# Optimization experiments

Measured on AMD Instinct MI355X. Metric: run time of the kernel, lower is better.

Reference implementation:

```python
import jax, jax.numpy as jnp
import numpy as np

B, S, D, H, HD, E, DE = 2, 512, 768, 12, 64, 50, 50  # batch, seq, input_dim, heads, head_dim, edge_dim, dep_embed_dim


def setup_inputs() -> dict:
    key = jax.random.key(0)
    ks = jax.random.split(key, 16)
    def xn(k, shape, s=0.02):
        return (jax.random.normal(k, shape, jnp.float32) * s)
    return {
        'weight_prob_softmax': jax.random.uniform(ks[0], (B, S, S, E), jnp.float32),
        'weight_adj': jax.random.normal(ks[1], (B, S, S, E), jnp.float32),
        'gcn_inputs': jax.random.normal(ks[2], (B, S, D), jnp.float32),
        'self_loop': jax.random.uniform(ks[3], (B, S, S, E), jnp.float32),
        # self.linear
        'W_lin': xn(ks[4], (D, D)), 'b_lin': jnp.zeros((D,), jnp.float32),
        # additive attention vectors fc_w1 / fc_w2 (stored [H, HD])
        'fc_w1': xn(ks[5], (H, HD), 0.2), 'fc_w2': xn(ks[6], (H, HD), 0.2),
        # edge_mlp: Linear(E,128) -> ReLU -> (Dropout eval) -> Linear(128,H)
        'We1': xn(ks[7], (128, E), 0.1), 'be1': jnp.zeros((128,), jnp.float32),
        'We2': xn(ks[8], (H, 128), 0.1), 'be2': jnp.zeros((H,), jnp.float32),
        # self.W output projection
        'W_out': xn(ks[9], (D, D)), 'b_out': jnp.zeros((D,), jnp.float32),
        # LayerNorm params
        'ln_a': jnp.ones((D,), jnp.float32), 'ln_b': jnp.zeros((D,), jnp.float32),
        # highway.W split into column blocks: [edge | edge_i | edge_j | node1 | node2]
        'Wh_e': xn(ks[10], (DE, E), 0.1), 'Wh_ei': xn(ks[11], (DE, E), 0.1),
        'Wh_ej': xn(ks[12], (DE, E), 0.1), 'Wh_n1': xn(ks[13], (DE, D), 0.05),
        'Wh_n2': xn(ks[14], (DE, D), 0.05), 'bh': jnp.zeros((DE,), jnp.float32),
    }


def reference(weight_prob_softmax, weight_adj, gcn_inputs, self_loop,
              W_lin, b_lin, fc_w1, fc_w2, We1, be1, We2, be2,
              W_out, b_out, ln_a, ln_b, Wh_e, Wh_ei, Wh_ej, Wh_n1, Wh_n2, bh):
    wps = self_loop + weight_prob_softmax                      # [B,S,S,E]
    mask = jnp.sum(wps, axis=-1) == 0.0                        # [B,S,S]
    feature = (gcn_inputs @ W_lin.T + b_lin).reshape(B, S, H, HD)
    attn_src = jnp.einsum('bshd,hd->bhs', feature, fc_w1)      # [B,H,S]
    attn_dst = jnp.einsum('bshd,hd->bhs', feature, fc_w2)      # [B,H,S]
    # edge MLP bias (dropout is identity in eval)
    hmid = jax.nn.relu(jnp.einsum('bije,fe->bijf', wps, We1) + be1)  # [B,S,S,128]
    A = jnp.einsum('bijf,hf->bhij', hmid, We2) + be2[None, :, None, None]  # [B,H,S,S]
    attn = jax.nn.leaky_relu(attn_src[:, :, :, None] + attn_dst[:, :, None, :] + A,
                             negative_slope=0.01)
    attn = jnp.where(mask[:, None, :, :], -jnp.inf, attn)
    attn = jax.nn.softmax(attn, axis=-1)
    gcn = jnp.einsum('bhij,bjhd->bihd', attn, feature).reshape(B, S, D)
    gcn = gcn @ W_out.T + b_out
    # torch LayerNorm variant: unbiased std, divide by (std + eps)
    mean = jnp.mean(gcn, axis=-1, keepdims=True)
    std = jnp.std(gcn, axis=-1, ddof=1, keepdims=True)
    gcn = ln_a * (gcn - mean) / (std + 1e-6) + ln_b
    node = jax.nn.relu(gcn)                                    # [B,S,D]
    # RefiningStrategy: W([edge, edge_i, edge_j, node1, node2]) via block matmuls
    ediag = jnp.diagonal(weight_adj, axis1=1, axis2=2).transpose(0, 2, 1)  # [B,S,E]
    edge_out = (jnp.einsum('bije,fe->bijf', weight_adj, Wh_e)
                + (ediag @ Wh_ei.T)[:, :, None, :]             # edge_i[b,i,j]=diag[b,i]
                + (ediag @ Wh_ej.T)[:, None, :, :]             # edge_j[b,i,j]=diag[b,j]
                + (node @ Wh_n1.T)[:, None, :, :]              # node1[b,i,j]=node[b,j]
                + (node @ Wh_n2.T)[:, :, None, :]              # node2[b,i,j]=node[b,i]
                + bh)                                          # [B,S,S,DE]
    return node, edge_out
```

## Files before the change

### kernel.cpp

```cpp
#include <hip/hip_runtime.h>
#include <math.h>
#include <stddef.h>

#define BB 2
#define SS 512
#define DD 768
#define HH 12
#define HDIM 64
#define EE 50
#define DE 50
#define F1 128

typedef float f32x4 __attribute__((ext_vector_type(4)));
typedef short s16x8 __attribute__((ext_vector_type(8)));

static __device__ __forceinline__ unsigned short f2bf(float x) {
  unsigned int u = __float_as_uint(x);
  unsigned int r = u + 0x7fffu + ((u >> 16) & 1u);
  return (unsigned short)(r >> 16);
}
static __device__ __forceinline__ float bf2f(unsigned short b) {
  return __uint_as_float(((unsigned int)b) << 16);
}

__global__ __launch_bounds__(256) void k_gemm_bias(
    const float* __restrict__ X, int ldx,
    const float* __restrict__ W,
    const float* __restrict__ bias,
    float* __restrict__ Y, int ldy,
    int M, int N, int K)
{
  __shared__ float Xs[32][68];
  __shared__ float Ws[32][68];
  int t = threadIdx.x;
  int tx = t & 15, ty = t >> 4;
  int m0 = blockIdx.y * 64, n0 = blockIdx.x * 64;
  float acc[4][4] = {};
  for (int k0 = 0; k0 < K; k0 += 32) {
#pragma unroll
    for (int q = 0; q < 2; ++q) {
      int idx = t + q * 256;
      int r = idx >> 3, c = (idx & 7) << 2;
      float4 v = *(const float4*)(X + (size_t)(m0 + r) * ldx + k0 + c);
      Xs[c + 0][r] = v.x; Xs[c + 1][r] = v.y; Xs[c + 2][r] = v.z; Xs[c + 3][r] = v.w;
      float4 w = *(const float4*)(W + (size_t)(n0 + r) * K + k0 + c);
      Ws[c + 0][r] = w.x; Ws[c + 1][r] = w.y; Ws[c + 2][r] = w.z; Ws[c + 3][r] = w.w;
    }
    __syncthreads();
#pragma unroll
    for (int kk = 0; kk < 32; ++kk) {
      float a[4], b[4];
#pragma unroll
      for (int u = 0; u < 4; ++u) a[u] = Xs[kk][ty * 4 + u];
#pragma unroll
      for (int u = 0; u < 4; ++u) b[u] = Ws[kk][tx * 4 + u];
#pragma unroll
      for (int i = 0; i < 4; ++i)
#pragma unroll
        for (int j = 0; j < 4; ++j) acc[i][j] += a[i] * b[j];
    }
    __syncthreads();
  }
#pragma unroll
  for (int i = 0; i < 4; ++i) {
    int m = m0 + ty * 4 + i;
#pragma unroll
    for (int j = 0; j < 4; ++j) {
      int n = n0 + tx * 4 + j;
      Y[(size_t)m * ldy + n] = acc[i][j] + bias[n];
    }
  }
}

__global__ __launch_bounds__(192) void k_attnvec(
    const float* __restrict__ feat, const float* __restrict__ w1,
    const float* __restrict__ w2, float* __restrict__ src, float* __restrict__ dst)
{
  int bs = blockIdx.x;
  int t = threadIdx.x;
  int h = t >> 4, l = t & 15;
  float4 f = *(const float4*)(feat + (size_t)bs * DD + h * HDIM + l * 4);
  float4 a = *(const float4*)(w1 + h * HDIM + l * 4);
  float4 c = *(const float4*)(w2 + h * HDIM + l * 4);
  float ps = f.x * a.x + f.y * a.y + f.z * a.z + f.w * a.w;
  float pd = f.x * c.x + f.y * c.y + f.z * c.z + f.w * c.w;
#pragma unroll
  for (int o = 8; o > 0; o >>= 1) {
    ps += __shfl_xor(ps, o);
    pd += __shfl_xor(pd, o);
  }
  if (l == 0) {
    int b = bs >> 9, s = bs & 511;
    src[((b * HH + h) << 9) + s] = ps;
    dst[((b * HH + h) << 9) + s] = pd;
  }
}

__global__ __launch_bounds__(64) void k_prep(
    const float* __restrict__ We1, const float* __restrict__ be1,
    const float* __restrict__ We2, const float* __restrict__ Whe,
    s16x8* __restrict__ wtab, float* __restrict__ betab,
    s16x8* __restrict__ wtabE)
{
  const int l = threadIdx.x;
  const int lr = l & 15, lg = l >> 4;
#pragma unroll
  for (int ks = 0; ks < 2; ++ks)
#pragma unroll
    for (int n = 0; n < 8; ++n) {
      s16x8 v;
#pragma unroll
      for (int u = 0; u < 8; ++u) {
        int e = ks * 32 + lg * 8 + u;
        float x = (e < 50) ? We1[(n * 16 + lr) * 50 + e] : 0.0f;
        v[u] = (short)f2bf(x);
      }
      wtab[(ks * 8 + n) * 64 + l] = v;
    }
#pragma unroll
  for (int kk = 0; kk < 4; ++kk) {
    s16x8 v;
#pragma unroll
    for (int u = 0; u < 8; ++u) {
      int f = kk * 32 + lg * 8 + u;
      v[u] = (short)((lr < 12) ? f2bf(We2[lr * 128 + f]) : (unsigned short)0);
    }
    wtab[(16 + kk) * 64 + l] = v;
  }
#pragma unroll
  for (int n = 0; n < 8; ++n) betab[n * 64 + l] = be1[n * 16 + lr];
#pragma unroll
  for (int nt = 0; nt < 4; ++nt)
#pragma unroll
    for (int ks = 0; ks < 2; ++ks) {
      int f = nt * 16 + lr;
      s16x8 v;
#pragma unroll
      for (int u = 0; u < 8; ++u) {
        int e = ks * 32 + lg * 8 + u;
        float x = (f < 50 && e < 50) ? Whe[f * 50 + e] : 0.0f;
        v[u] = (short)f2bf(x);
      }
      wtabE[(nt * 2 + ks) * 64 + l] = v;
    }
}

__global__ __launch_bounds__(256, 2) void k_fused_attn(
    const float* __restrict__ wprob, const float* __restrict__ sloop,
    const s16x8* __restrict__ wtab, const float* __restrict__ betab,
    const float* __restrict__ be2,
    const float* __restrict__ src, const float* __restrict__ dst,
    const float* __restrict__ feat, float* __restrict__ gout)
{
  __shared__ float p[2][12][512];
  __shared__ unsigned short hmid_s[128][72];
  __shared__ float masks[128];

  const int blk = blockIdx.x;
  const int b = blk >> 8;
  const int i0 = (blk & 255) << 1;
  const int t = threadIdx.x;
  const int w = t >> 6, l = t & 63;
  const int lr = l & 15, lg = l >> 4;
  const int jbase = w * 32;

  s16x8 wb[4];
#pragma unroll
  for (int kk = 0; kk < 4; ++kk) wb[kk] = wtab[(16 + kk) * 64 + l];
  float be1v[8];
#pragma unroll
  for (int n = 0; n < 8; ++n) be1v[n] = betab[n * 64 + l];
  const int hc = (lr < 12) ? lr : 0;
  const float be2v = be2[hc];
  const float srcv_[2] = {src[((b * HH + hc) << 9) + i0],
                          src[((b * HH + hc) << 9) + i0 + 1]};
  const float* drow = dst + ((size_t)(b * HH + hc) << 9);

  int offs[8];
  bool vmask[8];
#pragma unroll
  for (int s8 = 0; s8 < 8; ++s8) {
    int ks = s8 >> 2, q = s8 & 3;
    int off = ks * 32 + lg * 8 + 2 * q;
    vmask[s8] = (off <= 48);
    offs[s8] = vmask[s8] ? off : 0;
  }

#pragma unroll 2
  for (int it = 0; it < 8; ++it) {
    const int ii = it >> 2, c = it & 3;
    const int i = i0 + ii;
    const int j0c = c << 7;

    const size_t rowbase = ((size_t)(b * SS + i) * SS + j0c) * EE;
    float2 pA[2][8], pS[2][8];
#pragma unroll
    for (int jt = 0; jt < 2; ++jt) {
      const int jl = jbase + jt * 16 + lr;
      const float* wrow = wprob + rowbase + (size_t)jl * EE;
      const float* srow = sloop + rowbase + (size_t)jl * EE;
#pragma unroll
      for (int s8 = 0; s8 < 8; ++s8) {
        pA[jt][s8] = *(const float2*)(wrow + offs[s8]);
        pS[jt][s8] = *(const float2*)(srow + offs[s8]);
      }
    }
    float4 dv0 = *(const float4*)(drow + j0c + jbase + lg * 4);
    float4 dv1 = *(const float4*)(drow + j0c + jbase + 16 + lg * 4);

    s16x8 aA[2][2];
    float rsum[2];
#pragma unroll
    for (int jt = 0; jt < 2; ++jt) {
      float rs = 0.0f;
#pragma unroll
      for (int ks = 0; ks < 2; ++ks) {
        s16x8 f;
#pragma unroll
        for (int q = 0; q < 4; ++q) {
          int s8 = ks * 4 + q;
          float vx = vmask[s8] ? (pA[jt][s8].x + pS[jt][s8].x) : 0.0f;
          float vy = vmask[s8] ? (pA[jt][s8].y + pS[jt][s8].y) : 0.0f;
          f[2 * q] = (short)f2bf(vx);
          f[2 * q + 1] = (short)f2bf(vy);
          rs += vx + vy;
        }
        aA[jt][ks] = f;
      }
      rsum[jt] = rs;
    }
#pragma unroll
    for (int jt = 0; jt < 2; ++jt) {
      rsum[jt] += __shfl_xor(rsum[jt], 16);
      rsum[jt] += __shfl_xor(rsum[jt], 32);
    }
    if (lg == 0) {
      masks[jbase + lr] = (rsum[0] == 0.0f) ? 1.0f : 0.0f;
      masks[jbase + 16 + lr] = (rsum[1] == 0.0f) ? 1.0f : 0.0f;
    }

    f32x4 accB[2] = {};
#pragma unroll
    for (int h = 0; h < 2; ++h) {
      s16x8 wah[2][4];
#pragma unroll
      for (int ks = 0; ks < 2; ++ks)
#pragma unroll
        for (int nn = 0; nn < 4; ++nn)
          wah[ks][nn] = wtab[(ks * 8 + h * 4 + nn) * 64 + l];

      f32x4 accA[2][4] = {};
#pragma unroll
      for (int ks = 0; ks < 2; ++ks)
#pragma unroll
        for (int nn = 0; nn < 4; ++nn) {
          accA[0][nn] = __builtin_amdgcn_mfma_f32_16x16x32_bf16(aA[0][ks], wah[ks][nn], accA[0][nn], 0, 0, 0);
          accA[1][nn] = __builtin_amdgcn_mfma_f32_16x16x32_bf16(aA[1][ks], wah[ks][nn], accA[1][nn], 0, 0, 0);
        }
#pragma unroll
      for (int jt = 0; jt < 2; ++jt)
#pragma unroll
        for (int nn = 0; nn < 4; ++nn)
#pragma unroll
          for (int r = 0; r < 4; ++r) {
            float v = fmaxf(accA[jt][nn][r] + be1v[h * 4 + nn], 0.0f);
            hmid_s[jbase + jt * 16 + lg * 4 + r][nn * 16 + lr] = f2bf(v);
          }
#pragma unroll
      for (int kh = 0; kh < 2; ++kh) {
        int kk = 2 * h + kh;
        s16x8 a0 = *(const s16x8*)&hmid_s[jbase + lr][kh * 32 + lg * 8];
        s16x8 a1 = *(const s16x8*)&hmid_s[jbase + 16 + lr][kh * 32 + lg * 8];
        accB[0] = __builtin_amdgcn_mfma_f32_16x16x32_bf16(a0, wb[kk], accB[0], 0, 0, 0);
        accB[1] = __builtin_amdgcn_mfma_f32_16x16x32_bf16(a1, wb[kk], accB[1], 0, 0, 0);
      }
    }

    if (lr < 12) {
      const float srcv = srcv_[ii];
#pragma unroll
      for (int jt = 0; jt < 2; ++jt) {
        int jl = jbase + jt * 16 + lg * 4;
        const float4 dv = jt ? dv1 : dv0;
        float4 st;
#pragma unroll
        for (int r = 0; r < 4; ++r) {
          float x = accB[jt][r] + be2v + srcv + (&dv.x)[r];
          x = (x > 0.0f) ? x : 0.01f * x;
          if (masks[jl + r] != 0.0f) x = -INFINITY;
          (&st.x)[r] = x;
        }
        *(float4*)&p[ii][lr][j0c + jl] = st;
      }
    }
  }
  __syncthreads();

  for (int r = w; r < 24; r += 4) {
    int ii = r / 12, h = r % 12;
    float* row = p[ii][h];
    float vv[8];
    float m = -INFINITY;
#pragma unroll
    for (int u = 0; u < 8; ++u) {
      vv[u] = row[l + (u << 6)];
      m = fmaxf(m, vv[u]);
    }
#pragma unroll
    for (int o = 32; o > 0; o >>= 1) m = fmaxf(m, __shfl_xor(m, o));
    float s = 0.0f;
#pragma unroll
    for (int u = 0; u < 8; ++u) {
      float e = __expf(vv[u] - m);
      vv[u] = e;
      s += e;
    }
#pragma unroll
    for (int o = 32; o > 0; o >>= 1) s += __shfl_xor(s, o);
    float inv = 1.0f / s;
#pragma unroll
    for (int u = 0; u < 8; ++u) row[l + (u << 6)] = vv[u] * inv;
  }
  __syncthreads();

  float acc[2][3] = {};
  const float* fb = feat + (size_t)b * SS * DD;
  int h0 = t >> 6;
#pragma unroll 4
  for (int j = 0; j < 512; ++j) {
    const float* fr = fb + (size_t)j * DD;
    float f0 = fr[t], f1 = fr[t + 256], f2 = fr[t + 512];
    float p00 = p[0][h0][j], p10 = p[1][h0][j];
    float p01 = p[0][h0 + 4][j], p11 = p[1][h0 + 4][j];
    float p02 = p[0][h0 + 8][j], p12 = p[1][h0 + 8][j];
    acc[0][0] += p00 * f0; acc[0][1] += p01 * f1; acc[0][2] += p02 * f2;
    acc[1][0] += p10 * f0; acc[1][1] += p11 * f1; acc[1][2] += p12 * f2;
  }
#pragma unroll
  for (int ii = 0; ii < 2; ++ii)
#pragma unroll
    for (int u = 0; u < 3; ++u)
      gout[(size_t)(b * SS + i0 + ii) * DD + t + (u << 8)] = acc[ii][u];
}

__global__ __launch_bounds__(256) void k_ln(
    const float* __restrict__ gcn2, const float* __restrict__ ga,
    const float* __restrict__ gb, float* __restrict__ out)
{
  __shared__ float rs[4], rss[4];
  int row = blockIdx.x;
  int t = threadIdx.x;
  const float* x = gcn2 + (size_t)row * DD;
  float v[3];
  float s = 0.0f, ss2 = 0.0f;
#pragma unroll
  for (int u = 0; u < 3; ++u) {
    v[u] = x[t + (u << 8)];
    s += v[u];
    ss2 += v[u] * v[u];
  }
#pragma unroll
  for (int o = 32; o > 0; o >>= 1) {
    s += __shfl_down(s, o);
    ss2 += __shfl_down(ss2, o);
  }
  int w = t >> 6, l = t & 63;
  if (l == 0) { rs[w] = s; rss[w] = ss2; }
  __syncthreads();
  float S = rs[0] + rs[1] + rs[2] + rs[3];
  float SSum = rss[0] + rss[1] + rss[2] + rss[3];
  float mean = S * (1.0f / 768.0f);
  float var = (SSum - 768.0f * mean * mean) * (1.0f / 767.0f);
  var = fmaxf(var, 0.0f);
  float rinv = 1.0f / (sqrtf(var) + 1e-6f);
#pragma unroll
  for (int u = 0; u < 3; ++u) {
    int cidx = t + (u << 8);
    float y = ga[cidx] * (v[u] - mean) * rinv + gb[cidx];
    out[(size_t)row * DD + cidx] = fmaxf(y, 0.0f);
  }
}

__global__ __launch_bounds__(256) void k_pq(
    const float* __restrict__ node, const float* __restrict__ wadj,
    const float* __restrict__ Whei, const float* __restrict__ Whej,
    const float* __restrict__ Whn1, const float* __restrict__ Whn2,
    const float* __restrict__ bh, float* __restrict__ P, float* __restrict__ Q)
{
  __shared__ float nd[2][768];
  __shared__ float ed[2][64];
  const int bs0 = blockIdx.x * 2;
  const int t = threadIdx.x;
  const int w = t >> 6, l = t & 63;

  for (int q = t; q < 384; q += 256) {
    int rr = q / 192, idx = q % 192;
    *(float4*)(nd[rr] + idx * 4) =
        *(const float4*)(node + (size_t)(bs0 + rr) * DD + idx * 4);
  }
  {
    int rr = t >> 7, tt = t & 127;
    if (tt < 50) {
      int bs = bs0 + rr;
      int b = bs >> 9, s = bs & 511;
      ed[rr][tt] = wadj[((size_t)(b * SS + s) * SS + s) * EE + tt];
    }
  }
  __syncthreads();

  float4 n00 = *(const float4*)(nd[0] + l * 4);
  float4 n01 = *(const float4*)(nd[0] + 256 + l * 4);
  float4 n02 = *(const float4*)(nd[0] + 512 + l * 4);
  float4 n10 = *(const float4*)(nd[1] + l * 4);
  float4 n11 = *(const float4*)(nd[1] + 256 + l * 4);
  float4 n12 = *(const float4*)(nd[1] + 512 + l * 4);
  float el0 = (l < 50) ? ed[0][l] : 0.0f;
  float el1 = (l < 50) ? ed[1][l] : 0.0f;

  for (int o = w; o < 100; o += 4) {
    const int which = (o >= 50);
    const int f = o - which * 50;
    const float* Wn = which ? Whn1 : Whn2;
    const float* We = which ? Whej : Whei;
    const float* wr = Wn + f * DD;
    float4 w0 = *(const float4*)(wr + l * 4);
    float4 w1 = *(const float4*)(wr + 256 + l * 4);
    float4 w2 = *(const float4*)(wr + 512 + l * 4);
    float wev = (l < 50) ? We[f * EE + l] : 0.0f;
    float a0 = n00.x * w0.x + n00.y * w0.y + n00.z * w0.z + n00.w * w0.w
             + n01.x * w1.x + n01.y * w1.y + n01.z * w1.z + n01.w * w1.w
             + n02.x * w2.x + n02.y * w2.y + n02.z * w2.z + n02.w * w2.w
             + el0 * wev;
    float a1 = n10.x * w0.x + n10.y * w0.y + n10.z * w0.z + n10.w * w0.w
             + n11.x * w1.x + n11.y * w1.y + n11.z * w1.z + n11.w * w1.w
             + n12.x * w2.x + n12.y * w2.y + n12.z * w2.z + n12.w * w2.w
             + el1 * wev;
#pragma unroll
    for (int ofs = 32; ofs > 0; ofs >>= 1) {
      a0 += __shfl_xor(a0, ofs);
      a1 += __shfl_xor(a1, ofs);
    }
    if (l == 0) {
      float bias = which ? bh[f] : 0.0f;
      float* dst0 = (which ? Q : P) + (size_t)bs0 * DE + f;
      dst0[0] = a0 + bias;
      dst0[DE] = a1 + bias;
    }
  }
}

__global__ __launch_bounds__(256, 6) void k_edge_mfma(
    const float* __restrict__ wadj, const s16x8* __restrict__ wtabE,
    const float* __restrict__ P, const float* __restrict__ Q,
    float* __restrict__ eout)
{
  __shared__ __align__(16) unsigned char raw[25600];
  unsigned short (*adj_s)[72] = (unsigned short(*)[72])raw;
  float* park = (float*)raw;
  __shared__ float P_s[64];

  const int t = threadIdx.x;
  const size_t n0 = (size_t)blockIdx.x * 128;
  const int b = (int)(n0 >> 18);
  const int i = (int)((n0 & 262143) >> 9);
  const int j0 = (int)(n0 & 511);
  const int w = t >> 6, l = t & 63;
  const int lr = l & 15, lg = l >> 4;
  const int mbase = w * 32;

  float4 pw[7];
  {
    const float* wp = wadj + n0 * EE;
#pragma unroll
    for (int k = 0; k < 7; ++k)
      if (k < 6 || t < 64) pw[k] = *(const float4*)(wp + 4 * (t + 256 * k));
  }

  s16x8 we[4][2];
#pragma unroll
  for (int nt = 0; nt < 4; ++nt)
#pragma unroll
    for (int ks = 0; ks < 2; ++ks) we[nt][ks] = wtabE[(nt * 2 + ks) * 64 + l];
  if (t < 64) P_s[t] = (t < 50) ? P[(size_t)(b * SS + i) * DE + t] : 0.0f;

  for (int q = t; q < 896; q += 256) {
    int r = q / 7, cd = 25 + q % 7;
    ((unsigned int*)adj_s)[r * 36 + cd] = 0u;
  }

#pragma unroll
  for (int k = 0; k < 7; ++k)
    if (k < 6 || t < 64) {
      int f = 4 * (t + 256 * k);
      int j = f / 50;
      int e0 = f - j * 50;
#pragma unroll
      for (int u = 0; u < 4; ++u) {
        int e = e0 + u, jj = j;
        if (e >= 50) { e -= 50; jj += 1; }
        adj_s[jj][e] = f2bf((&pw[k].x)[u]);
      }
    }
  __syncthreads();

  f32x4 acc[2][4] = {};
#pragma unroll
  for (int ks = 0; ks < 2; ++ks) {
    s16x8 a0 = *(const s16x8*)&adj_s[mbase + lr][ks * 32 + lg * 8];
    s16x8 a1 = *(const s16x8*)&adj_s[mbase + 16 + lr][ks * 32 + lg * 8];
#pragma unroll
    for (int nt = 0; nt < 4; ++nt) {
      acc[0][nt] = __builtin_amdgcn_mfma_f32_16x16x32_bf16(a0, we[nt][ks], acc[0][nt], 0, 0, 0);
      acc[1][nt] = __builtin_amdgcn_mfma_f32_16x16x32_bf16(a1, we[nt][ks], acc[1][nt], 0, 0, 0);
    }
  }
  __syncthreads();

#pragma unroll
  for (int nt = 0; nt < 4; ++nt) {
    int f = nt * 16 + lr;
    if (f < 50) {
      float pf = P_s[f];
#pragma unroll
      for (int mt = 0; mt < 2; ++mt) {
        int m = mbase + mt * 16 + lg * 4;
        const float* qp = Q + (size_t)(b * SS + j0 + m) * DE + f;
#pragma unroll
        for (int r = 0; r < 4; ++r)
          park[(m + r) * DE + f] = acc[mt][nt][r] + pf + qp[r * DE];
      }
    }
  }
  __syncthreads();

  const float4* s4 = (const float4*)park;
  float4* d4 = (float4*)(eout + n0 * DE);
  for (int q = t; q < 1600; q += 256) d4[q] = s4[q];
}

extern "C" void kernel_launch(void* const* d_in, const int* in_sizes, int n_in,
                              void* d_out, int out_size, void* d_ws, size_t ws_size,
                              hipStream_t stream)
{
  const float* wprob = (const float*)d_in[0];
  const float* wadj  = (const float*)d_in[1];
  const float* gin   = (const float*)d_in[2];
  const float* sloop = (const float*)d_in[3];
  const float* W_lin = (const float*)d_in[4];
  const float* b_lin = (const float*)d_in[5];
  const float* fw1   = (const float*)d_in[6];
  const float* fw2   = (const float*)d_in[7];
  const float* We1   = (const float*)d_in[8];
  const float* be1   = (const float*)d_in[9];
  const float* We2   = (const float*)d_in[10];
  const float* be2   = (const float*)d_in[11];
  const float* W_out = (const float*)d_in[12];
  const float* b_out = (const float*)d_in[13];
  const float* ln_a  = (const float*)d_in[14];
  const float* ln_b  = (const float*)d_in[15];
  const float* Whe   = (const float*)d_in[16];
  const float* Whei  = (const float*)d_in[17];
  const float* Whej  = (const float*)d_in[18];
  const float* Whn1  = (const float*)d_in[19];
  const float* Whn2  = (const float*)d_in[20];
  const float* bh    = (const float*)d_in[21];

  float* ws = (float*)d_ws;
  float* feature = ws + 0;
  float* src     = ws + 786432;
  float* dst     = ws + 798720;
  float* gcnmid  = ws + 7102464;
  float* gcn2    = ws + 7888896;
  float* P       = ws + 8675328;
  float* Q       = ws + 8726528;
  s16x8* wtab    = (s16x8*)(ws + 8777728);
  float* betab   = ws + 8782848;
  s16x8* wtabE   = (s16x8*)(ws + 8783360);

  float* node = (float*)d_out;
  float* eout = (float*)d_out + 786432;

  k_prep<<<1, 64, 0, stream>>>(We1, be1, We2, Whe, wtab, betab, wtabE);
  k_gemm_bias<<<dim3(DD / 64, (BB * SS) / 64), 256, 0, stream>>>(
      gin, DD, W_lin, b_lin, feature, DD, BB * SS, DD, DD);
  k_attnvec<<<BB * SS, 192, 0, stream>>>(feature, fw1, fw2, src, dst);
  k_fused_attn<<<BB * SS / 2, 256, 0, stream>>>(
      wprob, sloop, wtab, betab, be2, src, dst, feature, gcnmid);
  k_gemm_bias<<<dim3(DD / 64, (BB * SS) / 64), 256, 0, stream>>>(
      gcnmid, DD, W_out, b_out, gcn2, DD, BB * SS, DD, DD);
  k_ln<<<BB * SS, 256, 0, stream>>>(gcn2, ln_a, ln_b, node);
  k_pq<<<BB * SS / 2, 256, 0, stream>>>(node, wadj, Whei, Whej, Whn1, Whn2, bh, P, Q);
  k_edge_mfma<<<(BB * SS * SS) / 128, 256, 0, stream>>>(wadj, wtabE, P, Q, eout);
}
```

Measured before the change: 301.9 us.

## Use bf16 MFMA for linear GEMMs and one query row per attention block

Replaces the fp32 SIMT tiled GEMM used for the input and output projections with a bf16 MFMA kernel that converts operands to bf16 while staging them in LDS. The fused attention kernel now handles one query row per block instead of two, which doubles the grid, halves the shared probability buffer and raises the occupancy hint to 3 blocks per CU. The aim is to cut GEMM compute time and improve latency hiding in the attention kernel. The cost is lower precision in the projections, and each feature row is now read once per query row instead of once per two rows, which increases global traffic in the aggregation loop.

Result: slower. 376.8 us (+24.8%).

```diff
diff --git a/kernel.cpp b/kernel.cpp
--- a/kernel.cpp
+++ b/kernel.cpp
@@ -13,6 +13,7 @@
 
 typedef float f32x4 __attribute__((ext_vector_type(4)));
 typedef short s16x8 __attribute__((ext_vector_type(8)));
+typedef unsigned short u16x4 __attribute__((ext_vector_type(4)));
 
 static __device__ __forceinline__ unsigned short f2bf(float x) {
   unsigned int u = __float_as_uint(x);
@@ -23,51 +24,54 @@
   return __uint_as_float(((unsigned int)b) << 16);
 }
 
-__global__ __launch_bounds__(256) void k_gemm_bias(
-    const float* __restrict__ X, int ldx,
+__global__ __launch_bounds__(256) void k_gemm_mfma(
+    const float* __restrict__ X,
     const float* __restrict__ W,
     const float* __restrict__ bias,
-    float* __restrict__ Y, int ldy,
-    int M, int N, int K)
-{
-  __shared__ float Xs[32][68];
-  __shared__ float Ws[32][68];
-  int t = threadIdx.x;
-  int tx = t & 15, ty = t >> 4;
-  int m0 = blockIdx.y * 64, n0 = blockIdx.x * 64;
-  float acc[4][4] = {};
-  for (int k0 = 0; k0 < K; k0 += 32) {
-#pragma unroll
-    for (int q = 0; q < 2; ++q) {
-      int idx = t + q * 256;
-      int r = idx >> 3, c = (idx & 7) << 2;
-      float4 v = *(const float4*)(X + (size_t)(m0 + r) * ldx + k0 + c);
-      Xs[c + 0][r] = v.x; Xs[c + 1][r] = v.y; Xs[c + 2][r] = v.z; Xs[c + 3][r] = v.w;
-      float4 w = *(const float4*)(W + (size_t)(n0 + r) * K + k0 + c);
-      Ws[c + 0][r] = w.x; Ws[c + 1][r] = w.y; Ws[c + 2][r] = w.z; Ws[c + 3][r] = w.w;
+    float* __restrict__ Y)
+{
+  __shared__ unsigned short Xs[64][72];
+  __shared__ unsigned short Wsh[64][72];
+  const int t = threadIdx.x;
+  const int w = t >> 6, l = t & 63;
+  const int lr = l & 15, lg = l >> 4;
+  const int n0 = blockIdx.x * 64, m0 = blockIdx.y * 64;
+
+  f32x4 acc[4] = {};
+  for (int k0 = 0; k0 < 768; k0 += 64) {
+#pragma unroll
+    for (int q = 0; q < 4; ++q) {
+      int fi = t + 256 * q;
+      int r = fi >> 4, c4 = (fi & 15) << 2;
+      float4 v = *(const float4*)(X + (size_t)(m0 + r) * 768 + k0 + c4);
+      u16x4 h;
+      h[0] = f2bf(v.x); h[1] = f2bf(v.y); h[2] = f2bf(v.z); h[3] = f2bf(v.w);
+      *(u16x4*)&Xs[r][c4] = h;
+      float4 wv = *(const float4*)(W + (size_t)(n0 + r) * 768 + k0 + c4);
+      u16x4 hw;
+      hw[0] = f2bf(wv.x); hw[1] = f2bf(wv.y); hw[2] = f2bf(wv.z); hw[3] = f2bf(wv.w);
+      *(u16x4*)&Wsh[r][c4] = hw;
     }
     __syncthreads();
 #pragma unroll
-    for (int kk = 0; kk < 32; ++kk) {
-      float a[4], b[4];
-#pragma unroll
-      for (int u = 0; u < 4; ++u) a[u] = Xs[kk][ty * 4 + u];
-#pragma unroll
-      for (int u = 0; u < 4; ++u) b[u] = Ws[kk][tx * 4 + u];
-#pragma unroll
-      for (int i = 0; i < 4; ++i)
-#pragma unroll
-        for (int j = 0; j < 4; ++j) acc[i][j] += a[i] * b[j];
+    for (int ks = 0; ks < 2; ++ks) {
+      s16x8 a = *(const s16x8*)&Xs[w * 16 + lr][ks * 32 + lg * 8];
+#pragma unroll
+      for (int nt = 0; nt < 4; ++nt) {
+        s16x8 bfr = *(const s16x8*)&Wsh[nt * 16 + lr][ks * 32 + lg * 8];
+        acc[nt] = __builtin_amdgcn_mfma_f32_16x16x32_bf16(a, bfr, acc[nt], 0, 0, 0);
+      }
     }
     __syncthreads();
   }
 #pragma unroll
-  for (int i = 0; i < 4; ++i) {
-    int m = m0 + ty * 4 + i;
-#pragma unroll
-    for (int j = 0; j < 4; ++j) {
-      int n = n0 + tx * 4 + j;
-      Y[(size_t)m * ldy + n] = acc[i][j] + bias[n];
+  for (int nt = 0; nt < 4; ++nt) {
+    int n = n0 + nt * 16 + lr;
+    float bv = bias[n];
+#pragma unroll
+    for (int r = 0; r < 4; ++r) {
+      int m = m0 + w * 16 + lg * 4 + r;
+      Y[(size_t)m * 768 + n] = acc[nt][r] + bv;
     }
   }
 }
@@ -145,20 +149,20 @@
     }
 }
 
-__global__ __launch_bounds__(256, 2) void k_fused_attn(
+__global__ __launch_bounds__(256, 3) void k_fused_attn(
     const float* __restrict__ wprob, const float* __restrict__ sloop,
     const s16x8* __restrict__ wtab, const float* __restrict__ betab,
     const float* __restrict__ be2,
     const float* __restrict__ src, const float* __restrict__ dst,
     const float* __restrict__ feat, float* __restrict__ gout)
 {
-  __shared__ float p[2][12][512];
+  __shared__ float p[12][512];
   __shared__ unsigned short hmid_s[128][72];
   __shared__ float masks[128];
 
-  const int blk = blockIdx.x;
-  const int b = blk >> 8;
-  const int i0 = (blk & 255) << 1;
+  const int bs = blockIdx.x;
+  const int b = bs >> 9;
+  const int i = bs & 511;
   const int t = threadIdx.x;
   const int w = t >> 6, l = t & 63;
   const int lr = l & 15, lg = l >> 4;
@@ -172,8 +176,7 @@
   for (int n = 0; n < 8; ++n) be1v[n] = betab[n * 64 + l];
   const int hc = (lr < 12) ? lr : 0;
   const float be2v = be2[hc];
-  const float srcv_[2] = {src[((b * HH + hc) << 9) + i0],
-                          src[((b * HH + hc) << 9) + i0 + 1]};
+  const float srcv = src[((b * HH + hc) << 9) + i];
   const float* drow = dst + ((size_t)(b * HH + hc) << 9);
 
   int offs[8];
@@ -186,10 +189,7 @@
     offs[s8] = vmask[s8] ? off : 0;
   }
 
-#pragma unroll 2
-  for (int it = 0; it < 8; ++it) {
-    const int ii = it >> 2, c = it & 3;
-    const int i = i0 + ii;
+  for (int c = 0; c < 4; ++c) {
     const int j0c = c << 7;
 
     const size_t rowbase = ((size_t)(b * SS + i) * SS + j0c) * EE;
@@ -277,7 +277,6 @@
     }
 
     if (lr < 12) {
-      const float srcv = srcv_[ii];
 #pragma unroll
       for (int jt = 0; jt < 2; ++jt) {
         int jl = jbase + jt * 16 + lg * 4;
@@ -290,15 +289,14 @@
           if (masks[jl + r] != 0.0f) x = -INFINITY;
           (&st.x)[r] = x;
         }
-        *(float4*)&p[ii][lr][j0c + jl] = st;
-      }
-    }
-  }
-  __syncthreads();
-
-  for (int r = w; r < 24; r += 4) {
-    int ii = r / 12, h = r % 12;
-    float* row = p[ii][h];
+        *(float4*)&p[lr][j0c + jl] = st;
+      }
+    }
+  }
+  __syncthreads();
+
+  for (int r = w; r < 12; r += 4) {
+    float* row = p[r];
     float vv[8];
     float m = -INFINITY;
 #pragma unroll
@@ -323,24 +321,20 @@
   }
   __syncthreads();
 
-  float acc[2][3] = {};
+  float acc[3] = {};
   const float* fb = feat + (size_t)b * SS * DD;
   int h0 = t >> 6;
 #pragma unroll 4
   for (int j = 0; j < 512; ++j) {
     const float* fr = fb + (size_t)j * DD;
     float f0 = fr[t], f1 = fr[t + 256], f2 = fr[t + 512];
-    float p00 = p[0][h0][j], p10 = p[1][h0][j];
-    float p01 = p[0][h0 + 4][j], p11 = p[1][h0 + 4][j];
-    float p02 = p[0][h0 + 8][j], p12 = p[1][h0 + 8][j];
-    acc[0][0] += p00 * f0; acc[0][1] += p01 * f1; acc[0][2] += p02 * f2;
-    acc[1][0] += p10 * f0; acc[1][1] += p11 * f1; acc[1][2] += p12 * f2;
-  }
-#pragma unroll
-  for (int ii = 0; ii < 2; ++ii)
-#pragma unroll
-    for (int u = 0; u < 3; ++u)
-      gout[(size_t)(b * SS + i0 + ii) * DD + t + (u << 8)] = acc[ii][u];
+    acc[0] += p[h0][j] * f0;
+    acc[1] += p[h0 + 4][j] * f1;
+    acc[2] += p[h0 + 8][j] * f2;
+  }
+#pragma unroll
+  for (int u = 0; u < 3; ++u)
+    gout[(size_t)bs * DD + t + (u << 8)] = acc[u];
 }
 
 __global__ __launch_bounds__(256) void k_ln(
@@ -581,13 +575,13 @@
   float* eout = (float*)d_out + 786432;
 
   k_prep<<<1, 64, 0, stream>>>(We1, be1, We2, Whe, wtab, betab, wtabE);
-  k_gemm_bias<<<dim3(DD / 64, (BB * SS) / 64), 256, 0, stream>>>(
-      gin, DD, W_lin, b_lin, feature, DD, BB * SS, DD, DD);
+  k_gemm_mfma<<<dim3(DD / 64, (BB * SS) / 64), 256, 0, stream>>>(
+      gin, W_lin, b_lin, feature);
   k_attnvec<<<BB * SS, 192, 0, stream>>>(feature, fw1, fw2, src, dst);
-  k_fused_attn<<<BB * SS / 2, 256, 0, stream>>>(
+  k_fused_attn<<<BB * SS, 256, 0, stream>>>(
       wprob, sloop, wtab, betab, be2, src, dst, feature, gcnmid);
-  k_gemm_bias<<<dim3(DD / 64, (BB * SS) / 64), 256, 0, stream>>>(
-      gcnmid, DD, W_out, b_out, gcn2, DD, BB * SS, DD, DD);
+  k_gemm_mfma<<<dim3(DD / 64, (BB * SS) / 64), 256, 0, stream>>>(
+      gcnmid, W_out, b_out, gcn2);
   k_ln<<<BB * SS, 256, 0, stream>>>(gcn2, ln_a, ln_b, node);
   k_pq<<<BB * SS / 2, 256, 0, stream>>>(node, wadj, Whei, Whej, Whn1, Whn2, bh, P, Q);
   k_edge_mfma<<<(BB * SS * SS) / 128, 256, 0, stream>>>(wadj, wtabE, P, Q, eout);
```
